# Kernel optimization log

Hardware: AMD Instinct MI355X
Metric: run time of the kernel (lower is better)

Reference implementation:

```python
import jax, jax.numpy as jnp
import numpy as np

B, C_IN, H, W = 4, 16, 64, 64
OUT_C, K, STRIDE = 32, 3, 1
NUM_DEG = 6   # numerator coeffs for x^0..x^5 (order[0]+1)
DEN_DEG = 4


def setup_inputs() -> dict:
    key = jax.random.key(0)
    k1, k2, k3 = jax.random.split(key, 3)
    x = jax.random.normal(k1, (B, C_IN, H, W), dtype=jnp.float32)
    nums = 0.1 * jax.random.normal(k2, (OUT_C * C_IN * K * K, NUM_DEG), dtype=jnp.float32)
    denoms = 0.1 * jax.random.normal(k3, (OUT_C * C_IN * K * K, DEN_DEG), dtype=jnp.float32)
    return {"input": x, "nums": nums, "denoms": denoms}


def _ka_conv(x, nums, denoms):
    pad = (K - 1) // 2
    xp = jnp.pad(x, ((0, 0), (0, 0), (pad, pad), (pad, pad)))
    Ho = (x.shape[2] + 2 * pad - K) // STRIDE + 1
    Wo = (x.shape[3] + 2 * pad - K) // STRIDE + 1
    # patches [B, C, K*K, Ho, Wo] ordered (c, ki, kj) to match nums row layout
    patches = jnp.stack(
        [xp[:, :, i:i + STRIDE * Ho:STRIDE, j:j + STRIDE * Wo:STRIDE]
         for i in range(K) for j in range(K)], axis=2)
    M = C_IN * K * K
    patches = patches.reshape(x.shape[0], M, Ho, Wo)
    # powers x^0..x^5 built by cumulative products (grad-safe at x=0)
    pows = [jnp.ones_like(patches)]
    for _ in range(NUM_DEG - 1):
        pows.append(pows[-1] * patches)
    pw = jnp.stack(pows, axis=-1)  # [B, M, Ho, Wo, NUM_DEG]
    a = nums.reshape(OUT_C, M, NUM_DEG)
    b = denoms.reshape(OUT_C, M, DEN_DEG)
    # per-weight rational: P/Q for every (out_channel, weight, position)
    num = jnp.einsum('bmhwp,omp->bomhw', pw, a)
    den = 1.0 + jnp.abs(jnp.einsum('bmhwq,omq->bomhw', pw[..., 1:1 + DEN_DEG], b))
    return jnp.sum(num / den, axis=2)  # [B, OUT_C, Ho, Wo]


def reference(input, nums, denoms):
    return _ka_conv(input, nums, denoms)
```

## Files before the change

### kernel.cpp

```cpp
#include <hip/hip_runtime.h>


constexpr int Bn = 4, Cin = 16, Hh = 64, Ww = 64, Oc = 32, Mtot = 144;

__global__ __launch_bounds__(256, 4)
void ka_conv_kernel(const float* __restrict__ x,
                    const float* __restrict__ nums,
                    const float* __restrict__ denoms,
                    float* __restrict__ out) {
  const int tid = threadIdx.x;
  int blk = blockIdx.x;
  const int ht = blk & 7;  blk >>= 3;
  const int o  = blk & 31; blk >>= 5;
  const int b  = blk;

  const int w  = tid & 63;
  const int rg = tid >> 6;
  const int h0 = ht * 8 + rg * 2;

  const int  wm   = max(w - 1, 0), wp = min(w + 1, Ww - 1);
  const bool wl   = (w - 1) >= 0;
  const bool wr   = (w + 1) < Ww;
  const int  h_1  = max(h0 - 1, 0);
  const int  h2c  = min(h0 + 2, Hh - 1);
  const bool htv  = (h0 - 1) >= 0;
  const bool hbv  = (h0 + 2) < Hh;
  const bool tl = htv && wl, tr_ = htv && wr;
  const bool bl = hbv && wl, br = hbv && wr;

  float acc0 = 0.f, acc1 = 0.f;
  const float* __restrict__ xb = x + (size_t)b * Cin * Hh * Ww;

  const float* __restrict__ anum = nums   + (size_t)o * Mtot * 6;
  const float* __restrict__ bden = denoms + (size_t)o * Mtot * 4;

#define TAP(t, vt, vb) do {                                                    \
    const float a0 = pa[(t)*6 + 0], a1 = pa[(t)*6 + 1], a2 = pa[(t)*6 + 2];    \
    const float a3 = pa[(t)*6 + 3], a4 = pa[(t)*6 + 4], a5 = pa[(t)*6 + 5];    \
    const float c1 = pb[(t)*4 + 0], c2 = pb[(t)*4 + 1];                        \
    const float c3 = pb[(t)*4 + 2], c4 = pb[(t)*4 + 3];                        \
    {                                                                          \
      const float v  = (vt);                                                   \
      float num = fmaf(fmaf(fmaf(fmaf(fmaf(a5,v,a4),v,a3),v,a2),v,a1),v,a0);   \
      float dp  = fmaf(fmaf(fmaf(c4,v,c3),v,c2),v,c1) * v;                     \
      float r   = __builtin_amdgcn_rcpf(1.0f + fabsf(dp));                     \
      acc0 = fmaf(num, r, acc0);                                               \
    }                                                                          \
    {                                                                          \
      const float v  = (vb);                                                   \
      float num = fmaf(fmaf(fmaf(fmaf(fmaf(a5,v,a4),v,a3),v,a2),v,a1),v,a0);   \
      float dp  = fmaf(fmaf(fmaf(c4,v,c3),v,c2),v,c1) * v;                     \
      float r   = __builtin_amdgcn_rcpf(1.0f + fabsf(dp));                     \
      acc1 = fmaf(num, r, acc1);                                               \
    }                                                                          \
  } while (0)

  #pragma unroll 2
  for (int c = 0; c < Cin; ++c) {
    const float* __restrict__ xc = xb + (size_t)c * (Hh * Ww);
    const float* __restrict__ r0 = xc + h_1 * Ww;
    const float* __restrict__ r1 = xc + h0 * Ww;
    const float* __restrict__ r2 = xc + (h0 + 1) * Ww;
    const float* __restrict__ r3 = xc + h2c * Ww;

    float v00 = r0[wm], v01 = r0[w], v02 = r0[wp];
    float v10 = r1[wm], v11 = r1[w], v12 = r1[wp];
    float v20 = r2[wm], v21 = r2[w], v22 = r2[wp];
    float v30 = r3[wm], v31 = r3[w], v32 = r3[wp];
    v00 = tl  ? v00 : 0.f;  v01 = htv ? v01 : 0.f;  v02 = tr_ ? v02 : 0.f;
    v10 = wl  ? v10 : 0.f;                          v12 = wr  ? v12 : 0.f;
    v20 = wl  ? v20 : 0.f;                          v22 = wr  ? v22 : 0.f;
    v30 = bl  ? v30 : 0.f;  v31 = hbv ? v31 : 0.f;  v32 = br  ? v32 : 0.f;

    const float* __restrict__ pa = anum + c * 54;
    const float* __restrict__ pb = bden + c * 36;
    TAP(0, v00, v10);  TAP(1, v01, v11);  TAP(2, v02, v12);
    TAP(3, v10, v20);  TAP(4, v11, v21);  TAP(5, v12, v22);
    TAP(6, v20, v30);  TAP(7, v21, v31);  TAP(8, v22, v32);
  }
#undef TAP

  float* op = out + ((size_t)(b * Oc + o) * Hh + h0) * Ww + w;
  op[0]  = acc0;
  op[Ww] = acc1;
}

extern "C" void kernel_launch(void* const* d_in, const int* in_sizes, int n_in,
                              void* d_out, int out_size, void* d_ws, size_t ws_size,
                              hipStream_t stream) {
  const float* x      = (const float*)d_in[0];
  const float* nums   = (const float*)d_in[1];
  const float* denoms = (const float*)d_in[2];
  float* out          = (float*)d_out;
  dim3 grid(Bn * Oc * 8);
  ka_conv_kernel<<<grid, 256, 0, stream>>>(x, nums, denoms, out);
}
```

Before: 33.84 us.

## Compute one output pixel per thread and double the grid

Each thread now produces one output row position instead of two, so the grid doubles to 2048 blocks. Block indices are reordered so the output channel varies fastest, meaning neighbouring blocks share the same input tile. The launch-bounds occupancy hint rises from 4 to 8. The cost is losing the reuse of shared input rows and weight loads across two outputs, so each output needs more loads.

```diff
diff --git a/kernel.cpp b/kernel.cpp
--- a/kernel.cpp
+++ b/kernel.cpp
@@ -3,86 +3,69 @@
 
 constexpr int Bn = 4, Cin = 16, Hh = 64, Ww = 64, Oc = 32, Mtot = 144;
 
-__global__ __launch_bounds__(256, 4)
+__global__ __launch_bounds__(256, 8)
 void ka_conv_kernel(const float* __restrict__ x,
                     const float* __restrict__ nums,
                     const float* __restrict__ denoms,
                     float* __restrict__ out) {
   const int tid = threadIdx.x;
-  int blk = blockIdx.x;
-  const int ht = blk & 7;  blk >>= 3;
-  const int o  = blk & 31; blk >>= 5;
-  const int b  = blk;
+  const int n   = blockIdx.x;
+  const int o   = n & 31;
+  const int ht  = (n >> 5) & 15;
+  const int b   = n >> 9;
 
   const int w  = tid & 63;
   const int rg = tid >> 6;
-  const int h0 = ht * 8 + rg * 2;
+  const int h  = ht * 4 + rg;
 
-  const int  wm   = max(w - 1, 0), wp = min(w + 1, Ww - 1);
-  const bool wl   = (w - 1) >= 0;
-  const bool wr   = (w + 1) < Ww;
-  const int  h_1  = max(h0 - 1, 0);
-  const int  h2c  = min(h0 + 2, Hh - 1);
-  const bool htv  = (h0 - 1) >= 0;
-  const bool hbv  = (h0 + 2) < Hh;
-  const bool tl = htv && wl, tr_ = htv && wr;
-  const bool bl = hbv && wl, br = hbv && wr;
+  const int  wm  = max(w - 1, 0), wp = min(w + 1, Ww - 1);
+  const bool wlv = w > 0, wrv = (w + 1) < Ww;
+  const int  hm  = max(h - 1, 0), hp = min(h + 1, Hh - 1);
+  const bool htv = h > 0, hbv = (h + 1) < Hh;
+  const bool m00 = htv && wlv, m01 = htv, m02 = htv && wrv;
+  const bool m10 = wlv,                    m12 = wrv;
+  const bool m20 = hbv && wlv, m21 = hbv, m22 = hbv && wrv;
 
-  float acc0 = 0.f, acc1 = 0.f;
-  const float* __restrict__ xb = x + (size_t)b * Cin * Hh * Ww;
-
+  float acc = 0.f;
+  const float* __restrict__ xb   = x + (size_t)b * Cin * Hh * Ww;
   const float* __restrict__ anum = nums   + (size_t)o * Mtot * 6;
   const float* __restrict__ bden = denoms + (size_t)o * Mtot * 4;
 
-#define TAP(t, vt, vb) do {                                                    \
+#define TAP(t, v_) do {                                                        \
     const float a0 = pa[(t)*6 + 0], a1 = pa[(t)*6 + 1], a2 = pa[(t)*6 + 2];    \
     const float a3 = pa[(t)*6 + 3], a4 = pa[(t)*6 + 4], a5 = pa[(t)*6 + 5];    \
     const float c1 = pb[(t)*4 + 0], c2 = pb[(t)*4 + 1];                        \
     const float c3 = pb[(t)*4 + 2], c4 = pb[(t)*4 + 3];                        \
-    {                                                                          \
-      const float v  = (vt);                                                   \
-      float num = fmaf(fmaf(fmaf(fmaf(fmaf(a5,v,a4),v,a3),v,a2),v,a1),v,a0);   \
-      float dp  = fmaf(fmaf(fmaf(c4,v,c3),v,c2),v,c1) * v;                     \
-      float r   = __builtin_amdgcn_rcpf(1.0f + fabsf(dp));                     \
-      acc0 = fmaf(num, r, acc0);                                               \
-    }                                                                          \
-    {                                                                          \
-      const float v  = (vb);                                                   \
-      float num = fmaf(fmaf(fmaf(fmaf(fmaf(a5,v,a4),v,a3),v,a2),v,a1),v,a0);   \
-      float dp  = fmaf(fmaf(fmaf(c4,v,c3),v,c2),v,c1) * v;                     \
-      float r   = __builtin_amdgcn_rcpf(1.0f + fabsf(dp));                     \
-      acc1 = fmaf(num, r, acc1);                                               \
-    }                                                                          \
+    const float v  = (v_);                                                     \
+    float num = fmaf(fmaf(fmaf(fmaf(fmaf(a5,v,a4),v,a3),v,a2),v,a1),v,a0);     \
+    float dp  = fmaf(fmaf(fmaf(c4,v,c3),v,c2),v,c1) * v;                       \
+    float r   = __builtin_amdgcn_rcpf(1.0f + fabsf(dp));                       \
+    acc = fmaf(num, r, acc);                                                   \
   } while (0)
 
   #pragma unroll 2
   for (int c = 0; c < Cin; ++c) {
     const float* __restrict__ xc = xb + (size_t)c * (Hh * Ww);
-    const float* __restrict__ r0 = xc + h_1 * Ww;
-    const float* __restrict__ r1 = xc + h0 * Ww;
-    const float* __restrict__ r2 = xc + (h0 + 1) * Ww;
-    const float* __restrict__ r3 = xc + h2c * Ww;
+    const float* __restrict__ r0 = xc + hm * Ww;
+    const float* __restrict__ r1 = xc + h * Ww;
+    const float* __restrict__ r2 = xc + hp * Ww;
 
     float v00 = r0[wm], v01 = r0[w], v02 = r0[wp];
     float v10 = r1[wm], v11 = r1[w], v12 = r1[wp];
     float v20 = r2[wm], v21 = r2[w], v22 = r2[wp];
-    float v30 = r3[wm], v31 = r3[w], v32 = r3[wp];
-    v00 = tl  ? v00 : 0.f;  v01 = htv ? v01 : 0.f;  v02 = tr_ ? v02 : 0.f;
-    v10 = wl  ? v10 : 0.f;                          v12 = wr  ? v12 : 0.f;
-    v20 = wl  ? v20 : 0.f;                          v22 = wr  ? v22 : 0.f;
-    v30 = bl  ? v30 : 0.f;  v31 = hbv ? v31 : 0.f;  v32 = br  ? v32 : 0.f;
+    v00 = m00 ? v00 : 0.f;  v01 = m01 ? v01 : 0.f;  v02 = m02 ? v02 : 0.f;
+    v10 = m10 ? v10 : 0.f;                          v12 = m12 ? v12 : 0.f;
+    v20 = m20 ? v20 : 0.f;  v21 = m21 ? v21 : 0.f;  v22 = m22 ? v22 : 0.f;
 
     const float* __restrict__ pa = anum + c * 54;
     const float* __restrict__ pb = bden + c * 36;
-    TAP(0, v00, v10);  TAP(1, v01, v11);  TAP(2, v02, v12);
-    TAP(3, v10, v20);  TAP(4, v11, v21);  TAP(5, v12, v22);
-    TAP(6, v20, v30);  TAP(7, v21, v31);  TAP(8, v22, v32);
+    TAP(0, v00);  TAP(1, v01);  TAP(2, v02);
+    TAP(3, v10);  TAP(4, v11);  TAP(5, v12);
+    TAP(6, v20);  TAP(7, v21);  TAP(8, v22);
   }
 #undef TAP
 
-  float* op = out + ((size_t)(b * Oc + o) * Hh + h0) * Ww + w;
-  op[0]  = acc0;
-  op[Ww] = acc1;
+  out[((size_t)(b * Oc + o) * Hh + h) * Ww + w] = acc;
 }
 
 extern "C" void kernel_launch(void* const* d_in, const int* in_sizes, int n_in,
@@ -92,6 +75,6 @@
   const float* nums   = (const float*)d_in[1];
   const float* denoms = (const float*)d_in[2];
   float* out          = (float*)d_out;
-  dim3 grid(Bn * Oc * 8);
+  dim3 grid(Bn * Oc * 16);
   ka_conv_kernel<<<grid, 256, 0, stream>>>(x, nums, denoms, out);
 }
```

Measured after the change: 40.76 us. +20.4%, slower.

## Split input channels across two thread halves with shared-memory reduction

Applied to the files above, without the earlier changes.

Each block now runs 512 threads, and the two halves each process 8 of the 16 input channels for the same output pixels. The partial sums are combined through shared memory before the store. This doubles the number of waves so the GPU has more parallelism to hide latency, since the grid of 1024 blocks of 256 threads was small. In exchange it adds a __syncthreads and an LDS round trip, and launch_bounds(512,8) may limit registers per thread.

```diff
diff --git a/kernel.cpp b/kernel.cpp
--- a/kernel.cpp
+++ b/kernel.cpp
@@ -3,34 +3,35 @@
 
 constexpr int Bn = 4, Cin = 16, Hh = 64, Ww = 64, Oc = 32, Mtot = 144;
 
-__global__ __launch_bounds__(256, 4)
+__global__ __launch_bounds__(512, 8)
 void ka_conv_kernel(const float* __restrict__ x,
                     const float* __restrict__ nums,
                     const float* __restrict__ denoms,
                     float* __restrict__ out) {
-  const int tid = threadIdx.x;
-  int blk = blockIdx.x;
-  const int ht = blk & 7;  blk >>= 3;
-  const int o  = blk & 31; blk >>= 5;
-  const int b  = blk;
+  __shared__ float part[512];
 
-  const int w  = tid & 63;
-  const int rg = tid >> 6;
+  const int tid  = threadIdx.x;
+  const int pix  = tid & 255;
+  const int half = tid >> 8;
+  const int n    = blockIdx.x;
+  const int ht   = n & 7;
+  const int o    = (n >> 3) & 31;
+  const int b    = n >> 8;
+
+  const int w  = pix & 63;
+  const int rg = pix >> 6;
   const int h0 = ht * 8 + rg * 2;
 
   const int  wm   = max(w - 1, 0), wp = min(w + 1, Ww - 1);
-  const bool wl   = (w - 1) >= 0;
-  const bool wr   = (w + 1) < Ww;
+  const bool wl   = w > 0, wr = (w + 1) < Ww;
   const int  h_1  = max(h0 - 1, 0);
   const int  h2c  = min(h0 + 2, Hh - 1);
-  const bool htv  = (h0 - 1) >= 0;
-  const bool hbv  = (h0 + 2) < Hh;
+  const bool htv  = h0 > 0, hbv = (h0 + 2) < Hh;
   const bool tl = htv && wl, tr_ = htv && wr;
   const bool bl = hbv && wl, br = hbv && wr;
 
   float acc0 = 0.f, acc1 = 0.f;
-  const float* __restrict__ xb = x + (size_t)b * Cin * Hh * Ww;
-
+  const float* __restrict__ xb   = x + (size_t)b * Cin * Hh * Ww;
   const float* __restrict__ anum = nums   + (size_t)o * Mtot * 6;
   const float* __restrict__ bden = denoms + (size_t)o * Mtot * 4;
 
@@ -55,8 +56,10 @@
     }                                                                          \
   } while (0)
 
+  const int cBeg = half * (Cin / 2);
   #pragma unroll 2
-  for (int c = 0; c < Cin; ++c) {
+  for (int ci = 0; ci < Cin / 2; ++ci) {
+    const int c = cBeg + ci;
     const float* __restrict__ xc = xb + (size_t)c * (Hh * Ww);
     const float* __restrict__ r0 = xc + h_1 * Ww;
     const float* __restrict__ r1 = xc + h0 * Ww;
@@ -80,9 +83,18 @@
   }
 #undef TAP
 
-  float* op = out + ((size_t)(b * Oc + o) * Hh + h0) * Ww + w;
-  op[0]  = acc0;
-  op[Ww] = acc1;
+  if (half == 1) {
+    part[pix]       = acc0;
+    part[pix + 256] = acc1;
+  }
+  __syncthreads();
+  if (half == 0) {
+    const float s0 = acc0 + part[pix];
+    const float s1 = acc1 + part[pix + 256];
+    float* op = out + ((size_t)(b * Oc + o) * Hh + h0) * Ww + w;
+    op[0]  = s0;
+    op[Ww] = s1;
+  }
 }
 
 extern "C" void kernel_launch(void* const* d_in, const int* in_sizes, int n_in,
@@ -93,5 +105,5 @@
   const float* denoms = (const float*)d_in[2];
   float* out          = (float*)d_out;
   dim3 grid(Bn * Oc * 8);
-  ka_conv_kernel<<<grid, 256, 0, stream>>>(x, nums, denoms, out);
+  ka_conv_kernel<<<grid, 512, 0, stream>>>(x, nums, denoms, out);
 }
```

Measured after the change: 134.1 us. 3.96x slower.
